# Kernel optimization log

Measured on AMD Instinct MI355X. Metric: run time of the kernel, lower is better.

Reference implementation:

```python
import jax, jax.numpy as jnp
import numpy as np

H = 8
HD = 16  # head_dim = out_features // n_heads = 128 // 8


def setup_inputs() -> dict:
    key = jax.random.key(0)
    k1, k2, k3, k4, k5 = jax.random.split(key, 5)
    B, N, F_IN, F_OUT = 4, 2048, 128, 128
    x = jax.random.normal(k1, (B, N, F_IN), dtype=jnp.float32)
    adj = jax.random.randint(k2, (B, N, N), 0, 2, dtype=jnp.int32)
    W = jax.random.normal(k3, (F_IN, F_OUT), dtype=jnp.float32) * (1.0 / np.sqrt(F_IN))
    a = jax.random.normal(k4, (H, 2 * HD), dtype=jnp.float32) * 0.1
    Wo = jax.random.normal(k5, (F_OUT, F_OUT), dtype=jnp.float32) * (1.0 / np.sqrt(F_OUT))
    bo = jnp.zeros((F_OUT,), dtype=jnp.float32)
    return {"x": x, "adj": adj, "W": W, "a": a, "Wo": Wo, "bo": bo}


def reference(x, adj, W, a, Wo, bo):
    B, N, _ = x.shape
    # Linear projection (no bias), split heads: [B,H,N,HD]
    Wx = (x @ W).reshape(B, N, H, HD).transpose(0, 2, 1, 3)
    # Additive attention scores: e_ij = leaky(a_l . Wx_i + a_r . Wx_j)
    e_i = jnp.einsum('bhnd,hd->bhn', Wx, a[:, :HD])  # [B,H,N]
    e_j = jnp.einsum('bhnd,hd->bhn', Wx, a[:, HD:])  # [B,H,N]
    e = jax.nn.leaky_relu(e_i[:, :, :, None] + e_j[:, :, None, :], negative_slope=0.2)
    # Mask to edges of adj; rows with no edges -> all -inf -> softmax NaN -> 0
    mask = (adj[:, None, :, :] == 0)  # [B,1,N,N] broadcast over heads
    e = jnp.where(mask, -jnp.inf, e)
    attn = jax.nn.softmax(e, axis=-1)
    attn = jnp.nan_to_num(attn, nan=0.0)
    # Weighted aggregation, merge heads: [B,N,F_OUT]
    h = jnp.einsum('bhij,bhjd->bhid', attn, Wx)
    h = h.transpose(0, 2, 1, 3).reshape(B, N, H * HD)
    # out_proj (nn.Linear: y = h @ Wo.T + bo) then ELU
    return jax.nn.elu(h @ Wo.T + bo)
```

## Files before the change

kernel.cpp:

```cpp
#include <hip/hip_runtime.h>
#include <hip/hip_bf16.h>
#include <cstdint>


typedef float f32x2 __attribute__((ext_vector_type(2)));
typedef float f32x4 __attribute__((ext_vector_type(4)));
typedef __bf16 bf16x8 __attribute__((ext_vector_type(8)));
typedef unsigned long long u64;

__device__ __forceinline__ float lsel(float v, u64 m, u64 lanebit) {
#if __has_builtin(__builtin_amdgcn_inverse_ballot_w64)
    (void)lanebit;
    return __builtin_amdgcn_inverse_ballot_w64(m) ? v : 0.0f;
#else
    return (m & lanebit) ? v : 0.0f;
#endif
}

__global__ __launch_bounds__(256)
void prep_kernel(const float* __restrict__ x, const float* __restrict__ W,
                 const float* __restrict__ a, const float* __restrict__ Wo,
                 const int* __restrict__ adj,
                 unsigned short* __restrict__ wxT,
                 float2* __restrict__ EI,
                 float* __restrict__ EjT, float* __restrict__ Ej5T,
                 float* __restrict__ WoT,
                 u64* __restrict__ tmask)
{
    const int t = threadIdx.x;

    if (blockIdx.x >= 1025) {
        __shared__ int al[16][257];
        const int blk2 = blockIdx.x - 1025;
        const int b = blk2 >> 9;
        const int tile = (blk2 >> 2) & 127;
        const int jq = blk2 & 3;
        const int rowbase = b * 2048 + tile * 16;
        const int w = t >> 6, lane = t & 63;
        const int r = lane & 15, jg = lane >> 4;
        const int srow = t >> 4, scol = (t & 15) * 16;

        #pragma unroll
        for (int cc = 0; cc < 2; ++cc) {
            const int jc = jq * 512 + cc * 256;
            const int* gsrc = adj + (size_t)(rowbase + srow) * 2048 + jc + scol;
            #pragma unroll
            for (int q = 0; q < 4; ++q) {
                const int4 v = *reinterpret_cast<const int4*>(&gsrc[q * 4]);
                al[srow][scol + q * 4 + 0] = v.x;
                al[srow][scol + q * 4 + 1] = v.y;
                al[srow][scol + q * 4 + 2] = v.z;
                al[srow][scol + q * 4 + 3] = v.w;
            }
            __syncthreads();
            u64 myw = 0;
            #pragma unroll
            for (int kk = 0; kk < 2; ++kk) {
                const int c0 = w * 64 + kk * 32 + jg * 8;
                const int4 a0 = *reinterpret_cast<const int4*>(&al[r][c0]);
                const int4 a1 = *reinterpret_cast<const int4*>(&al[r][c0 + 4]);
                const int av[8] = {a0.x, a0.y, a0.z, a0.w, a1.x, a1.y, a1.z, a1.w};
                #pragma unroll
                for (int e = 0; e < 8; ++e) {
                    const u64 bal = __ballot(av[e] != 0);
                    const int widx = kk * 8 + e;
                    if (lane == widx) myw = bal;
                }
            }
            __syncthreads();
            const int jtw = jq * 8 + cc * 4 + w;
            if (lane < 16)
                tmask[((size_t)(b * 128 + tile) * 32 + jtw) * 16 + lane] = myw;
        }
        return;
    }

    const int blk = blockIdx.x;
    if (blk == 1024) {
        if (t < 128)
            for (int k = 0; k < 128; ++k)
                WoT[k * 128 + t] = Wo[t * 128 + k];
        return;
    }
    __shared__ float xl[8 * 128];
    __shared__ float xw[8 * 128];
    const int row0 = blk * 8;
    if (t < 128) {
        #pragma unroll
        for (int r = 0; r < 8; ++r)
            xl[r * 128 + t] = x[(size_t)(row0 + r) * 128 + t];
    }
    __syncthreads();

    if (t < 128) {
        float acc[8] = {0.f, 0.f, 0.f, 0.f, 0.f, 0.f, 0.f, 0.f};
        for (int k = 0; k < 128; k += 4) {
            const float w0 = W[(k + 0) * 128 + t];
            const float w1 = W[(k + 1) * 128 + t];
            const float w2 = W[(k + 2) * 128 + t];
            const float w3 = W[(k + 3) * 128 + t];
            #pragma unroll
            for (int r = 0; r < 8; ++r) {
                const float4 xv = *reinterpret_cast<const float4*>(&xl[r * 128 + k]);
                acc[r] += xv.x * w0 + xv.y * w1 + xv.z * w2 + xv.w * w3;
            }
        }
        #pragma unroll
        for (int r = 0; r < 8; ++r) xw[r * 128 + t] = acc[r];
    }
    __syncthreads();

    if (t < 128) {
        const int b = row0 >> 11, n0 = row0 & 2047;
        bf16x8 st;
        #pragma unroll
        for (int r = 0; r < 8; ++r) st[r] = (__bf16)xw[r * 128 + t];
        *reinterpret_cast<bf16x8*>(&wxT[((size_t)(b * 128 + t)) * 2048 + n0]) = st;

        const int r = t >> 4, h = (t >> 1) & 7, s = t & 1;
        float dot = 0.f;
        #pragma unroll
        for (int d = 0; d < 16; ++d)
            dot += xw[r * 128 + h * 16 + d] * a[h * 32 + s * 16 + d];
        const float ef  = __expf(dot);
        const float ef5 = __expf(0.2f * dot);
        const int idx = (b * 8 + h) * 2048 + n0 + r;
        if (s) { EjT[idx] = ef; Ej5T[idx] = ef5; }
        else   { float2 ev; ev.x = ef; ev.y = ef5; EI[idx] = ev; }
    }
}

__global__ __launch_bounds__(512, 4)
void gat_kernel(const u64* __restrict__ tmask,
                const unsigned short* __restrict__ wxT,
                const float2* __restrict__ EI,
                const float* __restrict__ EjT, const float* __restrict__ Ej5T,
                const float* __restrict__ WoT, const float* __restrict__ bo,
                float* __restrict__ out)
{
    const int tid = threadIdx.x;
    const int h = tid >> 6;
    const int lane = tid & 63;
    const int r = lane & 15;
    const int jg = lane >> 4;
    const int jaof = jg * 8;
    const u64 lanebit = 1ull << lane;
    const int bid = (blockIdx.x & 7) * 64 + (blockIdx.x >> 3);
    const int b = bid >> 7;
    const int tile = bid & 127;
    const int ibase = tile << 4;

    __shared__ __align__(16) unsigned short VL[2][8][1024];
    __shared__ __align__(16) float EjL[2][8][64];
    __shared__ __align__(16) float Ej5L[2][8][64];
    __shared__ float hacc[16][128];

    const int eb = (b * 8 + h) * 2048;
    const float2 q0 = EI[eb + ibase + r];
    f32x2 EiE, Ei5E;
    EiE[0] = q0.x; EiE[1] = q0.x; Ei5E[0] = q0.y; Ei5E[1] = q0.y;
    const u64* tmrow = tmask + (size_t)(b * 128 + tile) * 512;

    const int h2 = tid >> 6, jj = tid & 63;
    const int uA = tid,        hA = uA >> 7, remA = uA & 127;
    const int fA = remA >> 3,  jbpA = remA & 7, jbA = jbpA ^ (fA & 7);
    const int uB = tid + 512,  hB = uB >> 7, remB = uB & 127;
    const int fB = remB >> 3,  jbpB = remB & 7, jbB = jbpB ^ (fB & 7);
    const unsigned short* wxb = wxT + (size_t)(b * 128) * 2048;
    const float* EjG  = EjT  + (b * 8 + h2) * 2048;
    const float* Ej5G = Ej5T + (b * 8 + h2) * 2048;

    f32x4 acc  = {0.f, 0.f, 0.f, 0.f};
    f32x4 accS = {0.f, 0.f, 0.f, 0.f};
    bf16x8 ones;
    #pragma unroll
    for (int e2 = 0; e2 < 8; ++e2) ones[e2] = (__bf16)1.0f;

    bf16x8 sv0, sv1; float se, se5;
    {
        const int j0 = 0;
        sv0 = *reinterpret_cast<const bf16x8*>(
                  &wxb[(size_t)(hA * 16 + fA) * 2048 + j0 + jbA * 8]);
        sv1 = *reinterpret_cast<const bf16x8*>(
                  &wxb[(size_t)(hB * 16 + fB) * 2048 + j0 + jbB * 8]);
        se  = EjG[j0 + jj];
        se5 = Ej5G[j0 + jj];
        *reinterpret_cast<bf16x8*>(&VL[0][hA][fA * 64 + jbpA * 8]) = sv0;
        *reinterpret_cast<bf16x8*>(&VL[0][hB][fB * 64 + jbpB * 8]) = sv1;
        EjL[0][h2][jj] = se;
        Ej5L[0][h2][jj] = se5;
    }
    __syncthreads();

    int cur = 0;
    for (int c = 0; c < 32; ++c) {
        const int j0n = ((c + 1) & 31) * 64;
        sv0 = *reinterpret_cast<const bf16x8*>(
                  &wxb[(size_t)(hA * 16 + fA) * 2048 + j0n + jbA * 8]);
        sv1 = *reinterpret_cast<const bf16x8*>(
                  &wxb[(size_t)(hB * 16 + fB) * 2048 + j0n + jbB * 8]);
        se  = EjG[j0n + jj];
        se5 = Ej5G[j0n + jj];
        __builtin_amdgcn_sched_barrier(0);

        const u64* tmw = tmrow + c * 16;
        u64 mw[16];
        #pragma unroll
        for (int e2 = 0; e2 < 16; ++e2) mw[e2] = tmw[e2];

        #pragma unroll
        for (int kk = 0; kk < 2; ++kk) {
            const float4 e0 = *reinterpret_cast<const float4*>(&EjL[cur][h][kk * 32 + jaof]);
            const float4 e1 = *reinterpret_cast<const float4*>(&EjL[cur][h][kk * 32 + jaof + 4]);
            const float4 f0 = *reinterpret_cast<const float4*>(&Ej5L[cur][h][kk * 32 + jaof]);
            const float4 f1 = *reinterpret_cast<const float4*>(&Ej5L[cur][h][kk * 32 + jaof + 4]);
            const int slot = r * 8 + (((kk << 2) | jg) ^ (r & 7));
            const bf16x8 v = *reinterpret_cast<const bf16x8*>(&VL[cur][h][slot * 8]);
            bf16x8 afr;
            #pragma unroll
            for (int ep = 0; ep < 4; ++ep) {
                const float4 ejv = (ep & 2) ? e1 : e0;
                const float4 ej5 = (ep & 2) ? f1 : f0;
                f32x2 ejp, ej5p;
                if (ep & 1) { ejp[0]=ejv.z; ejp[1]=ejv.w; ej5p[0]=ej5.z; ej5p[1]=ej5.w; }
                else        { ejp[0]=ejv.x; ejp[1]=ejv.y; ej5p[0]=ej5.x; ej5p[1]=ej5.y; }
                const f32x2 t1 = EiE * ejp;
                const f32x2 t2 = Ei5E * ej5p;
#if __has_builtin(__builtin_elementwise_max)
                const f32x2 tm2 = __builtin_elementwise_max(t1, t2);
#else
                f32x2 tm2; tm2[0] = fmaxf(t1[0], t2[0]); tm2[1] = fmaxf(t1[1], t2[1]);
#endif
                afr[2 * ep]     = (__bf16)lsel(tm2[0], mw[kk * 8 + 2 * ep],     lanebit);
                afr[2 * ep + 1] = (__bf16)lsel(tm2[1], mw[kk * 8 + 2 * ep + 1], lanebit);
            }
            acc  = __builtin_amdgcn_mfma_f32_16x16x32_bf16(afr, v,    acc,  0, 0, 0);
            accS = __builtin_amdgcn_mfma_f32_16x16x32_bf16(afr, ones, accS, 0, 0, 0);
        }

        const int nb = cur ^ 1;
        *reinterpret_cast<bf16x8*>(&VL[nb][hA][fA * 64 + jbpA * 8]) = sv0;
        *reinterpret_cast<bf16x8*>(&VL[nb][hB][fB * 64 + jbpB * 8]) = sv1;
        EjL[nb][h2][jj] = se;
        Ej5L[nb][h2][jj] = se5;
        __syncthreads();
        cur = nb;
    }

    #pragma unroll
    for (int q = 0; q < 4; ++q) {
        const int row = jg * 4 + q;
        const float inv = (accS[q] > 0.f) ? 1.f / accS[q] : 0.f;
        hacc[row][h * 16 + r] = acc[q] * inv;
    }
    __syncthreads();

    const int f = tid & 127;
    const int rg = tid >> 7;
    float o0 = 0.f, o1 = 0.f, o2 = 0.f, o3 = 0.f;
    for (int k = 0; k < 128; k += 4) {
        const float w0 = WoT[(k + 0) * 128 + f];
        const float w1 = WoT[(k + 1) * 128 + f];
        const float w2 = WoT[(k + 2) * 128 + f];
        const float w3 = WoT[(k + 3) * 128 + f];
        const float4 h0 = *reinterpret_cast<const float4*>(&hacc[rg * 4 + 0][k]);
        const float4 h1 = *reinterpret_cast<const float4*>(&hacc[rg * 4 + 1][k]);
        const float4 h2v = *reinterpret_cast<const float4*>(&hacc[rg * 4 + 2][k]);
        const float4 h3 = *reinterpret_cast<const float4*>(&hacc[rg * 4 + 3][k]);
        o0 += h0.x * w0 + h0.y * w1 + h0.z * w2 + h0.w * w3;
        o1 += h1.x * w0 + h1.y * w1 + h1.z * w2 + h1.w * w3;
        o2 += h2v.x * w0 + h2v.y * w1 + h2v.z * w2 + h2v.w * w3;
        o3 += h3.x * w0 + h3.y * w1 + h3.z * w2 + h3.w * w3;
    }
    const float bv = bo[f];
    float vv[4] = {o0 + bv, o1 + bv, o2 + bv, o3 + bv};
    #pragma unroll
    for (int q = 0; q < 4; ++q) {
        float v = vv[q];
        v = (v > 0.f) ? v : (__expf(v) - 1.f);
        out[(size_t)(b * 2048 + ibase + rg * 4 + q) * 128 + f] = v;
    }
}

extern "C" void kernel_launch(void* const* d_in, const int* in_sizes, int n_in,
                              void* d_out, int out_size, void* d_ws, size_t ws_size,
                              hipStream_t stream) {
    const float* x   = (const float*)d_in[0];
    const int*   adj = (const int*)d_in[1];
    const float* W   = (const float*)d_in[2];
    const float* a   = (const float*)d_in[3];
    const float* Wo  = (const float*)d_in[4];
    const float* bo  = (const float*)d_in[5];
    float* out = (float*)d_out;

    char* ws = (char*)d_ws;
    unsigned short* wxT = (unsigned short*)ws;
    float2* EI  = (float2*)(ws + (size_t)2 * 1024 * 1024);
    float* EjT  = (float*)(EI + 4 * 8 * 2048);
    float* Ej5T = EjT + 4 * 8 * 2048;
    float* WoT  = Ej5T + 4 * 8 * 2048;
    u64* tmask = (u64*)(WoT + 128 * 128);

    prep_kernel<<<dim3(1025 + 2048), dim3(256), 0, stream>>>(
        x, W, a, Wo, adj, wxT, EI, EjT, Ej5T, WoT, tmask);
    gat_kernel<<<dim3(512), dim3(512), 0, stream>>>(
        tmask, wxT, EI, EjT, Ej5T, WoT, bo, out);
}
```

Before: 68.67 us.

## Load value fragments directly into registers and widen attention chunks

The attention kernel no longer stages the projected features (V) through shared memory. Each wave now loads its own bf16 MFMA operand fragments straight from global memory into registers, double-buffered across iterations. The j-chunk grows from 64 to 128 columns, halving the number of loop iterations and block barriers, while only the Ej vectors stay in LDS. Separately, the prep kernel's block order is flipped so the adjacency-mask blocks are scheduled first. The last iteration's prefetch reads just past each row instead of wrapping around, and the design relies on uncoalesced per-wave global loads hitting in cache.

```diff
diff --git a/kernel.cpp b/kernel.cpp
--- a/kernel.cpp
+++ b/kernel.cpp
@@ -29,9 +29,9 @@
 {
     const int t = threadIdx.x;
 
-    if (blockIdx.x >= 1025) {
+    if (blockIdx.x < 2048) {
         __shared__ int al[16][257];
-        const int blk2 = blockIdx.x - 1025;
+        const int blk2 = blockIdx.x;
         const int b = blk2 >> 9;
         const int tile = (blk2 >> 2) & 127;
         const int jq = blk2 & 3;
@@ -75,7 +75,7 @@
         return;
     }
 
-    const int blk = blockIdx.x;
+    const int blk = blockIdx.x - 2048;
     if (blk == 1024) {
         if (t < 128)
             for (int k = 0; k < 128; ++k)
@@ -150,9 +150,8 @@
     const int tile = bid & 127;
     const int ibase = tile << 4;
 
-    __shared__ __align__(16) unsigned short VL[2][8][1024];
-    __shared__ __align__(16) float EjL[2][8][64];
-    __shared__ __align__(16) float Ej5L[2][8][64];
+    __shared__ __align__(16) float EjL[2][8][128];
+    __shared__ __align__(16) float Ej5L[2][8][128];
     __shared__ float hacc[16][128];
 
     const int eb = (b * 8 + h) * 2048;
@@ -161,14 +160,10 @@
     EiE[0] = q0.x; EiE[1] = q0.x; Ei5E[0] = q0.y; Ei5E[1] = q0.y;
     const u64* tmrow = tmask + (size_t)(b * 128 + tile) * 512;
 
-    const int h2 = tid >> 6, jj = tid & 63;
-    const int uA = tid,        hA = uA >> 7, remA = uA & 127;
-    const int fA = remA >> 3,  jbpA = remA & 7, jbA = jbpA ^ (fA & 7);
-    const int uB = tid + 512,  hB = uB >> 7, remB = uB & 127;
-    const int fB = remB >> 3,  jbpB = remB & 7, jbB = jbpB ^ (fB & 7);
-    const unsigned short* wxb = wxT + (size_t)(b * 128) * 2048;
-    const float* EjG  = EjT  + (b * 8 + h2) * 2048;
-    const float* Ej5G = Ej5T + (b * 8 + h2) * 2048;
+    const unsigned short* vrow = wxT + ((size_t)(b * 128 + h * 16 + r)) * 2048;
+    const int jj = lane;
+    const float* EjG  = EjT  + eb;
+    const float* Ej5G = Ej5T + eb;
 
     f32x4 acc  = {0.f, 0.f, 0.f, 0.f};
     f32x4 accS = {0.f, 0.f, 0.f, 0.f};
@@ -176,46 +171,47 @@
     #pragma unroll
     for (int e2 = 0; e2 < 8; ++e2) ones[e2] = (__bf16)1.0f;
 
-    bf16x8 sv0, sv1; float se, se5;
+    bf16x8 vC0, vC1, vC2, vC3, vN0, vN1, vN2, vN3;
+    vC0 = *reinterpret_cast<const bf16x8*>(&vrow[jaof]);
+    vC1 = *reinterpret_cast<const bf16x8*>(&vrow[32 + jaof]);
+    vC2 = *reinterpret_cast<const bf16x8*>(&vrow[64 + jaof]);
+    vC3 = *reinterpret_cast<const bf16x8*>(&vrow[96 + jaof]);
     {
-        const int j0 = 0;
-        sv0 = *reinterpret_cast<const bf16x8*>(
-                  &wxb[(size_t)(hA * 16 + fA) * 2048 + j0 + jbA * 8]);
-        sv1 = *reinterpret_cast<const bf16x8*>(
-                  &wxb[(size_t)(hB * 16 + fB) * 2048 + j0 + jbB * 8]);
-        se  = EjG[j0 + jj];
-        se5 = Ej5G[j0 + jj];
-        *reinterpret_cast<bf16x8*>(&VL[0][hA][fA * 64 + jbpA * 8]) = sv0;
-        *reinterpret_cast<bf16x8*>(&VL[0][hB][fB * 64 + jbpB * 8]) = sv1;
-        EjL[0][h2][jj] = se;
-        Ej5L[0][h2][jj] = se5;
+        const float2 s0 = *reinterpret_cast<const float2*>(&EjG[jj * 2]);
+        const float2 s1 = *reinterpret_cast<const float2*>(&Ej5G[jj * 2]);
+        *reinterpret_cast<float2*>(&EjL[0][h][jj * 2]) = s0;
+        *reinterpret_cast<float2*>(&Ej5L[0][h][jj * 2]) = s1;
     }
     __syncthreads();
 
     int cur = 0;
-    for (int c = 0; c < 32; ++c) {
-        const int j0n = ((c + 1) & 31) * 64;
-        sv0 = *reinterpret_cast<const bf16x8*>(
-                  &wxb[(size_t)(hA * 16 + fA) * 2048 + j0n + jbA * 8]);
-        sv1 = *reinterpret_cast<const bf16x8*>(
-                  &wxb[(size_t)(hB * 16 + fB) * 2048 + j0n + jbB * 8]);
-        se  = EjG[j0n + jj];
-        se5 = Ej5G[j0n + jj];
+    for (int c = 0; c < 16; ++c) {
+        const int jn = (c + 1) * 128;
+        vN0 = *reinterpret_cast<const bf16x8*>(&vrow[jn + jaof]);
+        vN1 = *reinterpret_cast<const bf16x8*>(&vrow[jn + 32 + jaof]);
+        vN2 = *reinterpret_cast<const bf16x8*>(&vrow[jn + 64 + jaof]);
+        vN3 = *reinterpret_cast<const bf16x8*>(&vrow[jn + 96 + jaof]);
+        const float2 sn  = *reinterpret_cast<const float2*>(&EjG[jn + jj * 2]);
+        const float2 sn5 = *reinterpret_cast<const float2*>(&Ej5G[jn + jj * 2]);
         __builtin_amdgcn_sched_barrier(0);
 
-        const u64* tmw = tmrow + c * 16;
-        u64 mw[16];
-        #pragma unroll
-        for (int e2 = 0; e2 < 16; ++e2) mw[e2] = tmw[e2];
-
-        #pragma unroll
-        for (int kk = 0; kk < 2; ++kk) {
-            const float4 e0 = *reinterpret_cast<const float4*>(&EjL[cur][h][kk * 32 + jaof]);
-            const float4 e1 = *reinterpret_cast<const float4*>(&EjL[cur][h][kk * 32 + jaof + 4]);
-            const float4 f0 = *reinterpret_cast<const float4*>(&Ej5L[cur][h][kk * 32 + jaof]);
-            const float4 f1 = *reinterpret_cast<const float4*>(&Ej5L[cur][h][kk * 32 + jaof + 4]);
-            const int slot = r * 8 + (((kk << 2) | jg) ^ (r & 7));
-            const bf16x8 v = *reinterpret_cast<const bf16x8*>(&VL[cur][h][slot * 8]);
+        const u64* tmw = tmrow + c * 32;
+        u64 mwA[16], mwB[16];
+        #pragma unroll
+        for (int e2 = 0; e2 < 16; ++e2) mwA[e2] = tmw[e2];
+        #pragma unroll
+        for (int e2 = 0; e2 < 16; ++e2) mwB[e2] = tmw[16 + e2];
+
+        #pragma unroll
+        for (int kk = 0; kk < 4; ++kk) {
+            const int jloc = kk * 32 + jaof;
+            const float4 e0 = *reinterpret_cast<const float4*>(&EjL[cur][h][jloc]);
+            const float4 e1 = *reinterpret_cast<const float4*>(&EjL[cur][h][jloc + 4]);
+            const float4 f0 = *reinterpret_cast<const float4*>(&Ej5L[cur][h][jloc]);
+            const float4 f1 = *reinterpret_cast<const float4*>(&Ej5L[cur][h][jloc + 4]);
+            const bf16x8 v = (kk == 0) ? vC0 : (kk == 1) ? vC1 : (kk == 2) ? vC2 : vC3;
+            const u64* mwp = (kk < 2) ? mwA : mwB;
+            const int mof = (kk & 1) * 8;
             bf16x8 afr;
             #pragma unroll
             for (int ep = 0; ep < 4; ++ep) {
@@ -231,19 +227,18 @@
 #else
                 f32x2 tm2; tm2[0] = fmaxf(t1[0], t2[0]); tm2[1] = fmaxf(t1[1], t2[1]);
 #endif
-                afr[2 * ep]     = (__bf16)lsel(tm2[0], mw[kk * 8 + 2 * ep],     lanebit);
-                afr[2 * ep + 1] = (__bf16)lsel(tm2[1], mw[kk * 8 + 2 * ep + 1], lanebit);
+                afr[2 * ep]     = (__bf16)lsel(tm2[0], mwp[mof + 2 * ep],     lanebit);
+                afr[2 * ep + 1] = (__bf16)lsel(tm2[1], mwp[mof + 2 * ep + 1], lanebit);
             }
             acc  = __builtin_amdgcn_mfma_f32_16x16x32_bf16(afr, v,    acc,  0, 0, 0);
             accS = __builtin_amdgcn_mfma_f32_16x16x32_bf16(afr, ones, accS, 0, 0, 0);
         }
 
         const int nb = cur ^ 1;
-        *reinterpret_cast<bf16x8*>(&VL[nb][hA][fA * 64 + jbpA * 8]) = sv0;
-        *reinterpret_cast<bf16x8*>(&VL[nb][hB][fB * 64 + jbpB * 8]) = sv1;
-        EjL[nb][h2][jj] = se;
-        Ej5L[nb][h2][jj] = se5;
+        *reinterpret_cast<float2*>(&EjL[nb][h][jj * 2]) = sn;
+        *reinterpret_cast<float2*>(&Ej5L[nb][h][jj * 2]) = sn5;
         __syncthreads();
+        vC0 = vN0; vC1 = vN1; vC2 = vN2; vC3 = vN3;
         cur = nb;
     }
 
@@ -301,7 +296,7 @@
     float* WoT  = Ej5T + 4 * 8 * 2048;
     u64* tmask = (u64*)(WoT + 128 * 128);
 
-    prep_kernel<<<dim3(1025 + 2048), dim3(256), 0, stream>>>(
+    prep_kernel<<<dim3(2048 + 1025), dim3(256), 0, stream>>>(
         x, W, a, Wo, adj, wxT, EI, EjT, Ej5T, WoT, tmask);
     gat_kernel<<<dim3(512), dim3(512), 0, stream>>>(
         tmask, wxT, EI, EjT, Ej5T, WoT, bo, out);
```

Result: slower. 72.38 us (+5.4%).
